# Kernel optimization log

Measured on AMD Instinct MI355X. Metric: run time of the kernel, lower is better.

## Reference

```python
import jax, jax.numpy as jnp
import numpy as np

IN_F = 256
OUT_F = 128
ALPHA = 0.02  # LeakyReLU negative slope
NEG_INF = -9e15


def setup_inputs() -> dict:
    key = jax.random.key(0)
    ks = jax.random.split(key, 6)
    N = 8192
    x = jax.random.normal(ks[0], (N, IN_F), dtype=jnp.float32)
    adj = jax.random.randint(ks[1], (N, N), 0, 2, dtype=jnp.int32)
    # nn.Linear(in_feature, out_feature)
    lim1 = 1.0 / np.sqrt(IN_F)
    W1 = jax.random.uniform(ks[2], (IN_F, OUT_F), minval=-lim1, maxval=lim1, dtype=jnp.float32)
    b1 = jax.random.uniform(ks[3], (OUT_F,), minval=-lim1, maxval=lim1, dtype=jnp.float32)
    # nn.Linear(2*out_feature, 1)
    lim2 = 1.0 / np.sqrt(2 * OUT_F)
    a = jax.random.uniform(ks[4], (2 * OUT_F,), minval=-lim2, maxval=lim2, dtype=jnp.float32)
    b_att = jax.random.uniform(ks[5], (), minval=-lim2, maxval=lim2, dtype=jnp.float32)
    return {"x": x, "adj": adj, "W1": W1, "b1": b1, "a": a, "b_att": b_att}


def reference(x, adj, W1, b1, a, b_att):
    # Wh = weight1(x)  -> [N, F_out]
    Wh = x @ W1 + b1
    # att(cat(Wh_i, Wh_j)) = Wh_i @ a[:F] + Wh_j @ a[F:] + b  (no N^2*2F tensor)
    f_src = Wh @ a[:OUT_F]   # [N]
    f_dst = Wh @ a[OUT_F:]   # [N]
    e = f_src[:, None] + f_dst[None, :] + b_att          # [N, N]
    e = jnp.where(e > 0, e, ALPHA * e)                    # LeakyReLU
    scores = jnp.where(adj > 0, e, NEG_INF)
    attention = jax.nn.softmax(scores, axis=1)            # [N, N]
    # dropout is identity in eval mode (training=False)
    h_prime = attention @ Wh                               # [N, F_out]
    return jax.nn.elu(h_prime)                             # concat=True
```

## Files before the change

### kernel.cpp

```cpp
#include <hip/hip_runtime.h>
#include <hip/hip_bf16.h>

#define NODES 8192
#define INF_ 256
#define OUTF 128
#define LRALPHA 0.02f

typedef __bf16 bf16;
typedef bf16 bf16x4 __attribute__((ext_vector_type(4)));
typedef bf16 bf16x8 __attribute__((ext_vector_type(8)));
typedef float f32x4 __attribute__((ext_vector_type(4)));
typedef float f32x16 __attribute__((ext_vector_type(16)));
typedef int i32x4 __attribute__((ext_vector_type(4)));

__global__ __launch_bounds__(256) void gat_prep_r4(
    const float* __restrict__ x, const float* __restrict__ W1,
    const float* __restrict__ b1, const float* __restrict__ a,
    const float* __restrict__ b_att,
    bf16* __restrict__ WhbT, float* __restrict__ E1,
    float* __restrict__ E2, float* __restrict__ F1, float* __restrict__ F2)
{
    __shared__ float xsT[64][36];
    __shared__ float ws1[64][132];
    __shared__ float wh[32][128];

    const int t = threadIdx.x;
    const int rbase = blockIdx.x * 32;
    const int tr = t >> 5;
    const int tc = t & 31;

    f32x4 acc[4];
    f32x4 bias = *(const f32x4*)&b1[tc * 4];
#pragma unroll
    for (int i = 0; i < 4; ++i) acc[i] = bias;

    for (int kt = 0; kt < 4; ++kt) {
        const int kb = kt * 64;
        {
            int r = t >> 3;
            int kq = (t & 7) * 8;
            f32x4 v0 = *(const f32x4*)&x[(size_t)(rbase + r) * INF_ + kb + kq];
            f32x4 v1 = *(const f32x4*)&x[(size_t)(rbase + r) * INF_ + kb + kq + 4];
#pragma unroll
            for (int i = 0; i < 4; ++i) xsT[kq + i][r] = v0[i];
#pragma unroll
            for (int i = 0; i < 4; ++i) xsT[kq + 4 + i][r] = v1[i];
        }
        {
            int kr = t >> 2;
            int cq = (t & 3) * 32;
#pragma unroll
            for (int i = 0; i < 8; ++i) {
                f32x4 v = *(const f32x4*)&W1[(size_t)(kb + kr) * OUTF + cq + i * 4];
                *(f32x4*)&ws1[kr][cq + i * 4] = v;
            }
        }
        __syncthreads();
        for (int kk = 0; kk < 64; ++kk) {
            f32x4 xa = *(const f32x4*)&xsT[kk][tr * 4];
            f32x4 wb = *(const f32x4*)&ws1[kk][tc * 4];
#pragma unroll
            for (int i = 0; i < 4; ++i)
#pragma unroll
                for (int j = 0; j < 4; ++j)
                    acc[i][j] += xa[i] * wb[j];
        }
        __syncthreads();
    }

#pragma unroll
    for (int i = 0; i < 4; ++i)
        *(f32x4*)&wh[tr * 4 + i][tc * 4] = acc[i];
    __syncthreads();

    if (t < 32) {
        float s1 = 0.f, s2 = 0.f;
        for (int c = 0; c < OUTF; ++c) {
            float v = wh[t][c];
            s1 += v * a[c];
            s2 += v * a[OUTF + c];
        }
        float fsv = s1 + b_att[0];
        int r = rbase + t;
        E1[r] = expf(fsv);
        E2[r] = expf(LRALPHA * fsv);
        F1[r] = expf(s2);
        F2[r] = expf(LRALPHA * s2);
    }

    {
        int c = t >> 1;
        int rr = (t & 1) * 16;
        bf16x8 b0, b1v;
#pragma unroll
        for (int i = 0; i < 8; ++i) b0[i] = (bf16)wh[rr + i][c];
#pragma unroll
        for (int i = 0; i < 8; ++i) b1v[i] = (bf16)wh[rr + 8 + i][c];
        *(bf16x8*)&WhbT[(size_t)c * NODES + rbase + rr] = b0;
        *(bf16x8*)&WhbT[(size_t)c * NODES + rbase + rr + 8] = b1v;
    }
}

#define SOFT_BAR() do { asm volatile("s_waitcnt lgkmcnt(0)" ::: "memory"); \
                        __builtin_amdgcn_s_barrier(); } while (0)

#define WBUF_OFF   0
#define DENRED_OFF 65536
#define F1T_OFF    66048
#define F2T_OFF    98816
#define ZONE_OFF   66048
#define SMEM2_SIZE 131584

__global__ __launch_bounds__(1024, 4) void gat_attn_r4(
    const int* __restrict__ adj,
    const bf16* __restrict__ WhbT,
    const float* __restrict__ E1, const float* __restrict__ E2,
    const float* __restrict__ F1, const float* __restrict__ F2,
    float* __restrict__ out)
{
    extern __shared__ char smem[];
    const int tid = threadIdx.x;
    const int lane = tid & 63;
    const int wv = tid >> 6;
    const int jg = wv >> 2;
    const int tt = wv & 3;
    const int rbase = blockIdx.x * 32;

    char* wbufA = smem + WBUF_OFF + jg * 16384;
    char* wbufB = wbufA + 8192;
    float* denred = (float*)(smem + DENRED_OFF);
    float* F1t = (float*)(smem + F1T_OFF);
    float* F2t = (float*)(smem + F2T_OFF);

    {
        int i = tid * 8;
        *(f32x4*)&F1t[i]     = *(const f32x4*)&F1[i];
        *(f32x4*)&F1t[i + 4] = *(const f32x4*)&F1[i + 4];
        *(f32x4*)&F2t[i]     = *(const f32x4*)&F2[i];
        *(f32x4*)&F2t[i + 4] = *(const f32x4*)&F2[i + 4];
    }

    const int r8 = lane >> 3;
    const int c8 = lane & 7;
    const int wrow = tt * 8 + r8;
    const int arow = lane & 31;
    const int ag = lane >> 5;

    const int gr = rbase + wrow;
    const float e1v = E1[gr];
    const float e2v = E2[gr];

    f32x16 acc;
#pragma unroll
    for (int i = 0; i < 16; ++i) acc[i] = 0.f;
    float den = 0.f;

    const int jw0 = jg * (NODES / 4);
    const size_t adj_row = (size_t)gr * NODES;
    const size_t whb_row = (size_t)(32 * tt + arow) * NODES;

    __syncthreads();

    auto compute_w = [&](char* buf, int jb, const i32x4* av) {
        const int cb = jb + c8 * 16;
#pragma unroll
        for (int h = 0; h < 2; ++h) {
            bf16x8 wb;
#pragma unroll
            for (int q = 0; q < 2; ++q) {
                f32x4 g1 = *(const f32x4*)&F1t[cb + h * 8 + q * 4];
                f32x4 g2 = *(const f32x4*)&F2t[cb + h * 8 + q * 4];
                i32x4 am = av[h * 2 + q];
#pragma unroll
                for (int jj = 0; jj < 4; ++jj) {
                    float tv = e1v * g1[jj];
                    float w = tv > 1.f ? tv : e2v * g2[jj];
                    w = am[jj] ? w : 0.f;
                    den += w;
                    wb[q * 4 + jj] = (bf16)w;
                }
            }
            const int off = (wrow * 256 + c8 * 32 + h * 16) ^ ((wrow & 7) << 4);
            *(bf16x8*)(buf + off) = wb;
        }
    };

    i32x4 ca[4], na[4];
#pragma unroll
    for (int q = 0; q < 4; ++q)
        ca[q] = *(const i32x4*)&adj[adj_row + jw0 + c8 * 16 + q * 4];
#pragma unroll
    for (int q = 0; q < 4; ++q)
        na[q] = *(const i32x4*)&adj[adj_row + jw0 + 128 + c8 * 16 + q * 4];
    compute_w(wbufA, jw0, ca);
    SOFT_BAR();

    char* cur = wbufA;
    char* nxt = wbufB;
#pragma unroll 2
    for (int p = 0; p < 16; ++p) {
        const int jb = jw0 + p * 128;

        bf16x8 wc[8];
#pragma unroll
        for (int m = 0; m < 8; ++m)
            wc[m] = *(const bf16x8*)&WhbT[whb_row + jb + 16 * m + 8 * ag];

        const int pc = (p + 2 <= 15) ? (p + 2) : 15;
        i32x4 fa[4];
#pragma unroll
        for (int q = 0; q < 4; ++q)
            fa[q] = *(const i32x4*)&adj[adj_row + jw0 + pc * 128 + c8 * 16 + q * 4];

        if (p < 15) compute_w(nxt, jb + 128, na);

#pragma unroll
        for (int m = 0; m < 8; ++m) {
            const int aoff = (arow * 256 + m * 32 + ag * 16) ^ ((arow & 7) << 4);
            bf16x8 af = *(const bf16x8*)(cur + aoff);
            acc = __builtin_amdgcn_mfma_f32_32x32x16_bf16(af, wc[m], acc, 0, 0, 0);
        }
        SOFT_BAR();
#pragma unroll
        for (int q = 0; q < 4; ++q) { na[q] = fa[q]; }
        char* tmp = cur; cur = nxt; nxt = tmp;
    }

    den += __shfl_xor(den, 1);
    den += __shfl_xor(den, 2);
    den += __shfl_xor(den, 4);
    if (c8 == 0) denred[jg * 32 + wrow] = den;

    if (jg > 0) {
        float* z = (float*)(smem + ZONE_OFF + (size_t)((jg - 1) * 4 + tt) * 4096) + lane * 16;
        *(f32x16*)z = acc;
    }
    __syncthreads();

    if (jg == 0) {
#pragma unroll
        for (int q = 0; q < 3; ++q) {
            const float* z = (const float*)(smem + ZONE_OFF + (size_t)(q * 4 + tt) * 4096) + lane * 16;
            f32x16 v = *(const f32x16*)z;
#pragma unroll
            for (int i = 0; i < 16; ++i) acc[i] += v[i];
        }
#pragma unroll
        for (int rg = 0; rg < 16; ++rg) {
            const int row = (rg & 3) + 8 * (rg >> 2) + 4 * ag;
            float ds = denred[row] + denred[32 + row] + denred[64 + row] + denred[96 + row];
            float v = acc[rg] / ds;
            v = v > 0.f ? v : expm1f(v);
            out[(size_t)(rbase + row) * OUTF + 32 * tt + arow] = v;
        }
    }
}

extern "C" void kernel_launch(void* const* d_in, const int* in_sizes, int n_in,
                              void* d_out, int out_size, void* d_ws, size_t ws_size,
                              hipStream_t stream) {
    const float* x     = (const float*)d_in[0];
    const int*   adj   = (const int*)d_in[1];
    const float* W1    = (const float*)d_in[2];
    const float* b1    = (const float*)d_in[3];
    const float* a     = (const float*)d_in[4];
    const float* b_att = (const float*)d_in[5];
    float* out = (float*)d_out;

    char* ws = (char*)d_ws;
    bf16* WhbT = (bf16*)ws;
    float* E1 = (float*)(ws + (size_t)2 * 1024 * 1024);
    float* E2 = E1 + NODES;
    float* F1 = E2 + NODES;
    float* F2 = F1 + NODES;

    hipLaunchKernelGGL(gat_prep_r4, dim3(NODES / 32), dim3(256), 0, stream,
                       x, W1, b1, a, b_att, WhbT, E1, E2, F1, F2);

    hipLaunchKernelGGL(gat_attn_r4, dim3(NODES / 32), dim3(1024), SMEM2_SIZE, stream,
                       adj, WhbT, E1, E2, F1, F2, out);
}
```

Before: 126.7 us.

## Compute attention weights in registers and feed MFMA directly, skipping LDS staging

Restructures the attention kernel so each wave computes its 32x16 attention-weight fragment in registers and uses it directly as the MFMA B operand. This removes the LDS double buffer and the per-iteration barriers. The j range is split across 8 strips of waves, each computing two 32x32 output tiles. Partial sums are combined with a tree reduction through a reused LDS zone. Shared memory drops to about 66KB, and the result is stored as vectorized rows. In exchange, every wave recomputes weights only for its own strip and holds two accumulators, which raises register pressure.

```diff
diff --git a/kernel.cpp b/kernel.cpp
--- a/kernel.cpp
+++ b/kernel.cpp
@@ -7,13 +7,12 @@
 #define LRALPHA 0.02f
 
 typedef __bf16 bf16;
-typedef bf16 bf16x4 __attribute__((ext_vector_type(4)));
 typedef bf16 bf16x8 __attribute__((ext_vector_type(8)));
 typedef float f32x4 __attribute__((ext_vector_type(4)));
 typedef float f32x16 __attribute__((ext_vector_type(16)));
 typedef int i32x4 __attribute__((ext_vector_type(4)));
 
-__global__ __launch_bounds__(256) void gat_prep_r4(
+__global__ __launch_bounds__(256) void gat_prep_r5(
     const float* __restrict__ x, const float* __restrict__ W1,
     const float* __restrict__ b1, const float* __restrict__ a,
     const float* __restrict__ b_att,
@@ -101,17 +100,12 @@
     }
 }
 
-#define SOFT_BAR() do { asm volatile("s_waitcnt lgkmcnt(0)" ::: "memory"); \
-                        __builtin_amdgcn_s_barrier(); } while (0)
-
-#define WBUF_OFF   0
-#define DENRED_OFF 65536
-#define F1T_OFF    66048
-#define F2T_OFF    98816
-#define ZONE_OFF   66048
-#define SMEM2_SIZE 131584
-
-__global__ __launch_bounds__(1024, 4) void gat_attn_r4(
+#define DENRED_OFF 0
+#define TAB_OFF    1024
+#define ZONE_OFF   1024
+#define SMEM2_SIZE (1024 + 65536)
+
+__global__ __launch_bounds__(1024, 4) void gat_attn_r5(
     const int* __restrict__ adj,
     const bf16* __restrict__ WhbT,
     const float* __restrict__ E1, const float* __restrict__ E2,
@@ -119,18 +113,19 @@
     float* __restrict__ out)
 {
     extern __shared__ char smem[];
+    float* denred = (float*)(smem + DENRED_OFF);
+    float* F1t = (float*)(smem + TAB_OFF);
+    float* F2t = (float*)(smem + TAB_OFF + 32768);
+    char* zones = smem + ZONE_OFF;
+
     const int tid = threadIdx.x;
     const int lane = tid & 63;
     const int wv = tid >> 6;
-    const int jg = wv >> 2;
-    const int tt = wv & 3;
+    const int strip = wv >> 1;
+    const int mh = wv & 1;
     const int rbase = blockIdx.x * 32;
-
-    char* wbufA = smem + WBUF_OFF + jg * 16384;
-    char* wbufB = wbufA + 8192;
-    float* denred = (float*)(smem + DENRED_OFF);
-    float* F1t = (float*)(smem + F1T_OFF);
-    float* F2t = (float*)(smem + F2T_OFF);
+    const int r = lane & 31;
+    const int ag = lane >> 5;
 
     {
         int i = tid * 8;
@@ -140,118 +135,115 @@
         *(f32x4*)&F2t[i + 4] = *(const f32x4*)&F2[i + 4];
     }
 
-    const int r8 = lane >> 3;
-    const int c8 = lane & 7;
-    const int wrow = tt * 8 + r8;
-    const int arow = lane & 31;
-    const int ag = lane >> 5;
-
-    const int gr = rbase + wrow;
-    const float e1v = E1[gr];
-    const float e2v = E2[gr];
-
-    f32x16 acc;
-#pragma unroll
-    for (int i = 0; i < 16; ++i) acc[i] = 0.f;
+    const float e1v = E1[rbase + r];
+    const float e2v = E2[rbase + r];
+    const size_t adj_row = (size_t)(rbase + r) * NODES;
+    const int j00 = strip * 1024;
+    const size_t wrow0 = (size_t)(r + 64 * mh) * NODES;
+    const size_t wrow1 = wrow0 + (size_t)32 * NODES;
+
+    f32x16 acc0, acc1;
+#pragma unroll
+    for (int i = 0; i < 16; ++i) { acc0[i] = 0.f; acc1[i] = 0.f; }
     float den = 0.f;
 
-    const int jw0 = jg * (NODES / 4);
-    const size_t adj_row = (size_t)gr * NODES;
-    const size_t whb_row = (size_t)(32 * tt + arow) * NODES;
-
-    __syncthreads();
-
-    auto compute_w = [&](char* buf, int jb, const i32x4* av) {
-        const int cb = jb + c8 * 16;
-#pragma unroll
-        for (int h = 0; h < 2; ++h) {
-            bf16x8 wb;
-#pragma unroll
-            for (int q = 0; q < 2; ++q) {
-                f32x4 g1 = *(const f32x4*)&F1t[cb + h * 8 + q * 4];
-                f32x4 g2 = *(const f32x4*)&F2t[cb + h * 8 + q * 4];
-                i32x4 am = av[h * 2 + q];
-#pragma unroll
-                for (int jj = 0; jj < 4; ++jj) {
-                    float tv = e1v * g1[jj];
-                    float w = tv > 1.f ? tv : e2v * g2[jj];
-                    w = am[jj] ? w : 0.f;
-                    den += w;
-                    wb[q * 4 + jj] = (bf16)w;
-                }
+    __syncthreads();
+
+    i32x4 ca0 = *(const i32x4*)&adj[adj_row + j00 + ag * 8];
+    i32x4 ca1 = *(const i32x4*)&adj[adj_row + j00 + ag * 8 + 4];
+    i32x4 na0 = *(const i32x4*)&adj[adj_row + j00 + 16 + ag * 8];
+    i32x4 na1 = *(const i32x4*)&adj[adj_row + j00 + 16 + ag * 8 + 4];
+    bf16x8 wc0 = *(const bf16x8*)&WhbT[wrow0 + j00 + ag * 8];
+    bf16x8 wc1 = *(const bf16x8*)&WhbT[wrow1 + j00 + ag * 8];
+
+#pragma unroll 4
+    for (int s = 0; s < 64; ++s) {
+        const int jl = j00 + s * 16 + ag * 8;
+        const int sc = (s + 2 <= 63) ? (s + 2) : 63;
+        const int sw = (s + 1 <= 63) ? (s + 1) : 63;
+        i32x4 fa0 = *(const i32x4*)&adj[adj_row + j00 + sc * 16 + ag * 8];
+        i32x4 fa1 = *(const i32x4*)&adj[adj_row + j00 + sc * 16 + ag * 8 + 4];
+        bf16x8 wn0 = *(const bf16x8*)&WhbT[wrow0 + j00 + sw * 16 + ag * 8];
+        bf16x8 wn1 = *(const bf16x8*)&WhbT[wrow1 + j00 + sw * 16 + ag * 8];
+
+        f32x4 g1a = *(const f32x4*)&F1t[jl];
+        f32x4 g1b = *(const f32x4*)&F1t[jl + 4];
+        f32x4 g2a = *(const f32x4*)&F2t[jl];
+        f32x4 g2b = *(const f32x4*)&F2t[jl + 4];
+
+        bf16x8 wb;
+#pragma unroll
+        for (int jj = 0; jj < 4; ++jj) {
+            float tv = e1v * g1a[jj];
+            float w = tv > 1.f ? tv : e2v * g2a[jj];
+            w = ca0[jj] ? w : 0.f;
+            den += w;
+            wb[jj] = (bf16)w;
+        }
+#pragma unroll
+        for (int jj = 0; jj < 4; ++jj) {
+            float tv = e1v * g1b[jj];
+            float w = tv > 1.f ? tv : e2v * g2b[jj];
+            w = ca1[jj] ? w : 0.f;
+            den += w;
+            wb[4 + jj] = (bf16)w;
+        }
+
+        acc0 = __builtin_amdgcn_mfma_f32_32x32x16_bf16(wc0, wb, acc0, 0, 0, 0);
+        acc1 = __builtin_amdgcn_mfma_f32_32x32x16_bf16(wc1, wb, acc1, 0, 0, 0);
+
+        ca0 = na0; ca1 = na1; na0 = fa0; na1 = fa1;
+        wc0 = wn0; wc1 = wn1;
+    }
+
+    den += __shfl_xor(den, 32);
+
+    __syncthreads();
+    if (mh == 0 && lane < 32) denred[strip * 32 + lane] = den;
+
+    auto dump = [&](int slot) {
+        float* z = (float*)(zones + (size_t)slot * 8192) + lane * 32;
+        *(f32x16*)z = acc0;
+        *(f32x16*)(z + 16) = acc1;
+    };
+    auto take = [&](int slot) {
+        const float* z = (const float*)(zones + (size_t)slot * 8192) + lane * 32;
+        f32x16 v0 = *(const f32x16*)z;
+        f32x16 v1 = *(const f32x16*)(z + 16);
+#pragma unroll
+        for (int i = 0; i < 16; ++i) { acc0[i] += v0[i]; acc1[i] += v1[i]; }
+    };
+
+    if (strip >= 4) dump((strip - 4) * 2 + mh);
+    __syncthreads();
+    if (strip < 4) take(strip * 2 + mh);
+    __syncthreads();
+    if (strip == 2 || strip == 3) dump((strip - 2) * 2 + mh);
+    __syncthreads();
+    if (strip < 2) take(strip * 2 + mh);
+    __syncthreads();
+    if (strip == 1) dump(mh);
+    __syncthreads();
+
+    if (strip == 0) {
+        take(mh);
+        float ds = 0.f;
+#pragma unroll
+        for (int w = 0; w < 8; ++w) ds += denred[w * 32 + r];
+        const float inv = 1.f / ds;
+#pragma unroll
+        for (int u = 0; u < 4; ++u) {
+            f32x4 o0, o1;
+#pragma unroll
+            for (int e = 0; e < 4; ++e) {
+                float v0 = acc0[4 * u + e] * inv;
+                float v1 = acc1[4 * u + e] * inv;
+                o0[e] = v0 > 0.f ? v0 : expm1f(v0);
+                o1[e] = v1 > 0.f ? v1 : expm1f(v1);
             }
-            const int off = (wrow * 256 + c8 * 32 + h * 16) ^ ((wrow & 7) << 4);
-            *(bf16x8*)(buf + off) = wb;
-        }
-    };
-
-    i32x4 ca[4], na[4];
-#pragma unroll
-    for (int q = 0; q < 4; ++q)
-        ca[q] = *(const i32x4*)&adj[adj_row + jw0 + c8 * 16 + q * 4];
-#pragma unroll
-    for (int q = 0; q < 4; ++q)
-        na[q] = *(const i32x4*)&adj[adj_row + jw0 + 128 + c8 * 16 + q * 4];
-    compute_w(wbufA, jw0, ca);
-    SOFT_BAR();
-
-    char* cur = wbufA;
-    char* nxt = wbufB;
-#pragma unroll 2
-    for (int p = 0; p < 16; ++p) {
-        const int jb = jw0 + p * 128;
-
-        bf16x8 wc[8];
-#pragma unroll
-        for (int m = 0; m < 8; ++m)
-            wc[m] = *(const bf16x8*)&WhbT[whb_row + jb + 16 * m + 8 * ag];
-
-        const int pc = (p + 2 <= 15) ? (p + 2) : 15;
-        i32x4 fa[4];
-#pragma unroll
-        for (int q = 0; q < 4; ++q)
-            fa[q] = *(const i32x4*)&adj[adj_row + jw0 + pc * 128 + c8 * 16 + q * 4];
-
-        if (p < 15) compute_w(nxt, jb + 128, na);
-
-#pragma unroll
-        for (int m = 0; m < 8; ++m) {
-            const int aoff = (arow * 256 + m * 32 + ag * 16) ^ ((arow & 7) << 4);
-            bf16x8 af = *(const bf16x8*)(cur + aoff);
-            acc = __builtin_amdgcn_mfma_f32_32x32x16_bf16(af, wc[m], acc, 0, 0, 0);
-        }
-        SOFT_BAR();
-#pragma unroll
-        for (int q = 0; q < 4; ++q) { na[q] = fa[q]; }
-        char* tmp = cur; cur = nxt; nxt = tmp;
-    }
-
-    den += __shfl_xor(den, 1);
-    den += __shfl_xor(den, 2);
-    den += __shfl_xor(den, 4);
-    if (c8 == 0) denred[jg * 32 + wrow] = den;
-
-    if (jg > 0) {
-        float* z = (float*)(smem + ZONE_OFF + (size_t)((jg - 1) * 4 + tt) * 4096) + lane * 16;
-        *(f32x16*)z = acc;
-    }
-    __syncthreads();
-
-    if (jg == 0) {
-#pragma unroll
-        for (int q = 0; q < 3; ++q) {
-            const float* z = (const float*)(smem + ZONE_OFF + (size_t)(q * 4 + tt) * 4096) + lane * 16;
-            f32x16 v = *(const f32x16*)z;
-#pragma unroll
-            for (int i = 0; i < 16; ++i) acc[i] += v[i];
-        }
-#pragma unroll
-        for (int rg = 0; rg < 16; ++rg) {
-            const int row = (rg & 3) + 8 * (rg >> 2) + 4 * ag;
-            float ds = denred[row] + denred[32 + row] + denred[64 + row] + denred[96 + row];
-            float v = acc[rg] / ds;
-            v = v > 0.f ? v : expm1f(v);
-            out[(size_t)(rbase + row) * OUTF + 32 * tt + arow] = v;
+            const int cbase = 8 * u + 4 * ag;
+            *(f32x4*)&out[(size_t)(rbase + r) * OUTF + 64 * mh + cbase] = o0;
+            *(f32x4*)&out[(size_t)(rbase + r) * OUTF + 64 * mh + 32 + cbase] = o1;
         }
     }
 }
@@ -274,9 +266,9 @@
     float* F1 = E2 + NODES;
     float* F2 = F1 + NODES;
 
-    hipLaunchKernelGGL(gat_prep_r4, dim3(NODES / 32), dim3(256), 0, stream,
+    hipLaunchKernelGGL(gat_prep_r5, dim3(NODES / 32), dim3(256), 0, stream,
                        x, W1, b1, a, b_att, WhbT, E1, E2, F1, F2);
 
-    hipLaunchKernelGGL(gat_attn_r4, dim3(NODES / 32), dim3(1024), SMEM2_SIZE, stream,
+    hipLaunchKernelGGL(gat_attn_r5, dim3(NODES / 32), dim3(1024), SMEM2_SIZE, stream,
                        adj, WhbT, E1, E2, F1, F2, out);
 }
```

Result: slower. 188.7 us (+48.9%).
